# Kernel tuning notes

Measured on AMD Instinct MI355X. Metric: run time of the kernel, lower is better.

The kernel has to match this reference:

```python
import jax, jax.numpy as jnp
import numpy as np

FEAT_DIM = 128
TIME_DIM = 128
D_MODEL = FEAT_DIM + TIME_DIM  # 256
N_HEAD = 2
D_K = D_MODEL // N_HEAD  # 128
B, N = 4096, 64


def setup_inputs() -> dict:
    key = jax.random.key(0)
    ks = jax.random.split(key, 16)
    s = lambda k, sh, sc=0.05: jax.random.normal(k, sh, dtype=jnp.float32) * sc
    return {
        "src": jax.random.normal(ks[0], (B, FEAT_DIM), dtype=jnp.float32),
        "src_t": jax.random.normal(ks[1], (B, 1, TIME_DIM), dtype=jnp.float32),
        "seq": jax.random.normal(ks[2], (B, N, FEAT_DIM), dtype=jnp.float32),
        "seq_t": jax.random.normal(ks[3], (B, N, TIME_DIM), dtype=jnp.float32),
        "mask": jax.random.randint(ks[4], (B, N), 0, 2).astype(jnp.bool_),
        # attention params (x @ W convention, W: [d_model, n_head*d_k])
        "w_qs": s(ks[5], (D_MODEL, N_HEAD * D_K)),
        "w_ks": s(ks[6], (D_MODEL, N_HEAD * D_K)),
        "w_vs": s(ks[7], (D_MODEL, N_HEAD * D_K)),
        "fc_w": s(ks[8], (N_HEAD * D_K, D_MODEL)),
        "fc_b": jnp.zeros((D_MODEL,), jnp.float32),
        "ln_g": jnp.ones((D_MODEL,), jnp.float32),
        "ln_b": jnp.zeros((D_MODEL,), jnp.float32),
        # MergeLayer params: fc1 [(d_model+feat), feat], fc2 [feat, feat]
        "fc1_w": s(ks[9], (D_MODEL + FEAT_DIM, FEAT_DIM)),
        "fc1_b": jnp.zeros((FEAT_DIM,), jnp.float32),
        "fc2_w": s(ks[10], (FEAT_DIM, FEAT_DIM)),
        "fc2_b": jnp.zeros((FEAT_DIM,), jnp.float32),
    }


def _layer_norm(x, g, b, eps=1e-5):
    mu = jnp.mean(x, axis=-1, keepdims=True)
    var = jnp.mean((x - mu) ** 2, axis=-1, keepdims=True)
    return (x - mu) * jax.lax.rsqrt(var + eps) * g + b


def reference(src, src_t, seq, seq_t, mask,
              w_qs, w_ks, w_vs, fc_w, fc_b, ln_g, ln_b,
              fc1_w, fc1_b, fc2_w, fc2_b):
    # q: [B,1,D_MODEL] = cat(src, src_t); k=v: [B,N,D_MODEL]
    q_in = jnp.concatenate([src[:, None, :], src_t], axis=2)
    k_in = jnp.concatenate([seq, seq_t], axis=2)

    q = (q_in @ w_qs).reshape(B, 1, N_HEAD, D_K)   # [B,1,H,dk]
    k = (k_in @ w_ks).reshape(B, N, N_HEAD, D_K)   # [B,N,H,dk]
    v = (k_in @ w_vs).reshape(B, N, N_HEAD, D_K)   # [B,N,H,dv]

    # scaled dot-product attention, len_q == 1
    attn = jnp.einsum('bqhd,bkhd->bhqk', q, k) / jnp.sqrt(jnp.float32(D_K))
    attn = jnp.where(mask[:, None, None, :], jnp.float32(-1e10), attn)
    attn = jax.nn.softmax(attn, axis=-1)           # [B,H,1,N]

    out = jnp.einsum('bhqk,bkhd->bqhd', attn, v).reshape(B, 1, N_HEAD * D_K)
    out = out @ fc_w + fc_b                         # dropout is identity (eval)
    out = _layer_norm(out + q_in, ln_g, ln_b)       # [B,1,D_MODEL]

    out = out[:, 0, :]                              # squeeze -> [B,D_MODEL]
    # MergeLayer: cat(out, src) -> fc1 -> relu -> fc2
    h = jnp.concatenate([out, src], axis=1)
    h = jax.nn.relu(h @ fc1_w + fc1_b)
    merged = h @ fc2_w + fc2_b                      # [B, FEAT_DIM]

    # attn squeeze: [n_head*B, N] ordering matches torch view(n_head, B, ...)
    attn_sq = jnp.transpose(attn[:, :, 0, :], (1, 0, 2)).reshape(N_HEAD * B, N)
    return merged, attn_sq
```

## Files before the change

### kernel.cpp

```cpp
#include <hip/hip_runtime.h>


__device__ __forceinline__ void fma4(float4& a, float s, const float4& w) {
  a.x = fmaf(s, w.x, a.x); a.y = fmaf(s, w.y, a.y);
  a.z = fmaf(s, w.z, a.z); a.w = fmaf(s, w.w, a.w);
}
__device__ __forceinline__ float dot4(const float4& a, const float4& b) {
  return a.x * b.x + a.y * b.y + a.z * b.z + a.w * b.w;
}

__global__ __launch_bounds__(256) void k_wf(const float* __restrict__ w_qs,
                                            const float* __restrict__ w_ks,
                                            float* __restrict__ W) {
  const int idx = blockIdx.x * 256 + threadIdx.x;
  const int c = idx >> 9;
  const int col = idx & 511;
  const int h = col >> 8;
  const int j = col & 255;
  const float* a = w_qs + c * 256 + h * 128;
  const float* bk = w_ks + j * 256 + h * 128;
  float acc = 0.f;
#pragma unroll
  for (int d = 0; d < 128; d += 4)
    acc += dot4(*(const float4*)&a[d], *(const float4*)&bk[d]);
  W[idx] = acc * 0.08838834764831845f;
}

__global__ __launch_bounds__(256) void k_qk(const float* __restrict__ src,
                                            const float* __restrict__ srct,
                                            const float* __restrict__ W,
                                            float* __restrict__ QK) {
  __shared__ float sQ[16 * 256];
  const int tid = threadIdx.x;
  const int rb = (blockIdx.x >> 1) * 16;
  const int ch = (blockIdx.x & 1) * 256;
  {
    const int r = tid >> 4;
    const int cb = (tid & 15) * 16;
#pragma unroll
    for (int i = 0; i < 4; ++i) {
      const int c = cb + i * 4;
      float4 v = (c < 128) ? *(const float4*)&src[(rb + r) * 128 + c]
                           : *(const float4*)&srct[(rb + r) * 128 + (c - 128)];
      *(float4*)&sQ[r * 256 + c] = v;
    }
  }
  __syncthreads();
  const int rg = tid >> 6;
  const int cg = tid & 63;
  const int col = ch + cg * 4;
  float4 acc[4] = {};
  for (int k = 0; k < 256; k += 4) {
    const float4 w0 = *(const float4*)&W[(k + 0) * 512 + col];
    const float4 w1 = *(const float4*)&W[(k + 1) * 512 + col];
    const float4 w2 = *(const float4*)&W[(k + 2) * 512 + col];
    const float4 w3 = *(const float4*)&W[(k + 3) * 512 + col];
#pragma unroll
    for (int r = 0; r < 4; ++r) {
      const float4 a = *(const float4*)&sQ[(rg * 4 + r) * 256 + k];
      fma4(acc[r], a.x, w0); fma4(acc[r], a.y, w1);
      fma4(acc[r], a.z, w2); fma4(acc[r], a.w, w3);
    }
  }
#pragma unroll
  for (int r = 0; r < 4; ++r)
    *(float4*)&QK[(rb + rg * 4 + r) * 512 + col] = acc[r];
}

__global__ __launch_bounds__(256) void k_attn(const float* __restrict__ seq,
                                              const float* __restrict__ seqt,
                                              const unsigned int* __restrict__ mw,
                                              float* QKS,
                                              float* __restrict__ att) {
  __shared__ float sqk[512];
  __shared__ float part0[4][64];
  __shared__ float part1[4][64];
  __shared__ float sa0[64];
  __shared__ float sa1[64];
  __shared__ int nlist[64];
  const int tid = threadIdx.x;
  const int lane = tid & 63;
  const int w = tid >> 6;
  const int b = blockIdx.x;

  if (tid < 128)
    *(float4*)&sqk[tid * 4] = *(const float4*)&QKS[b * 512 + tid * 4];
  const bool masked = (mw[b * 64 + lane] != 0u);
  __syncthreads();

  const float* rowp = (w < 2) ? (seq + b * 8192 + lane * 128 + w * 64)
                              : (seqt + b * 8192 + lane * 128 + (w - 2) * 64);
  float p0 = 0.f, p1 = 0.f;
  if (!masked) {
    const float* q0 = &sqk[w * 64];
    const float* q1 = &sqk[256 + w * 64];
#pragma unroll 8
    for (int i = 0; i < 16; ++i) {
      const float4 kv = *(const float4*)&rowp[i * 4];
      p0 += dot4(kv, *(const float4*)&q0[i * 4]);
      p1 += dot4(kv, *(const float4*)&q1[i * 4]);
    }
  }
  part0[w][lane] = p0;
  part1[w][lane] = p1;
  __syncthreads();

  const float fp0 =
      part0[0][lane] + part0[1][lane] + part0[2][lane] + part0[3][lane];
  const float fp1 =
      part1[0][lane] + part1[1][lane] + part1[2][lane] + part1[3][lane];
  const float e0 = masked ? 0.f : __expf(fp0);
  const float e1 = masked ? 0.f : __expf(fp1);
  float l0 = e0, l1 = e1;
#pragma unroll
  for (int off = 32; off >= 1; off >>= 1) {
    l0 += __shfl_xor(l0, off);
    l1 += __shfl_xor(l1, off);
  }
  const float a0 = e0 / l0;
  const float a1 = e1 / l1;
  const unsigned long long bits = __ballot(!masked);
  if (w == 0) {
    att[b * 64 + lane] = a0;
    att[4096 * 64 + b * 64 + lane] = a1;
    sa0[lane] = a0;
    sa1[lane] = a1;
    const int pos = __popcll(bits & ((1ull << lane) - 1ull));
    if (!masked) nlist[pos] = lane;
  }
  __syncthreads();

  const int cnt = __popcll(bits);
  const float* kin2 = (w < 2) ? (seq + b * 8192 + w * 64 + lane)
                              : (seqt + b * 8192 + (w - 2) * 64 + lane);
  float s0 = 0.f, s1 = 0.f;
  int t = 0;
  for (; t + 4 <= cnt; t += 4) {
    const int n0 = nlist[t + 0];
    const int n1 = nlist[t + 1];
    const int n2 = nlist[t + 2];
    const int n3 = nlist[t + 3];
    const float k0 = kin2[n0 * 128];
    const float k1 = kin2[n1 * 128];
    const float k2 = kin2[n2 * 128];
    const float k3 = kin2[n3 * 128];
    s0 = fmaf(sa0[n0], k0, s0); s1 = fmaf(sa1[n0], k0, s1);
    s0 = fmaf(sa0[n1], k1, s0); s1 = fmaf(sa1[n1], k1, s1);
    s0 = fmaf(sa0[n2], k2, s0); s1 = fmaf(sa1[n2], k2, s1);
    s0 = fmaf(sa0[n3], k3, s0); s1 = fmaf(sa1[n3], k3, s1);
  }
  for (; t < cnt; ++t) {
    const int n = nlist[t];
    const float kv = kin2[n * 128];
    s0 = fmaf(sa0[n], kv, s0);
    s1 = fmaf(sa1[n], kv, s1);
  }
  QKS[b * 512 + w * 64 + lane] = s0;
  QKS[b * 512 + 256 + w * 64 + lane] = s1;
}

__global__ __launch_bounds__(256) void k_epi(
    const float* __restrict__ S, const float* __restrict__ src,
    const float* __restrict__ srct, const float* __restrict__ w_vs,
    const float* __restrict__ fc_w, const float* __restrict__ fc_b,
    const float* __restrict__ ln_g, const float* __restrict__ ln_b,
    const float* __restrict__ fc1_w, const float* __restrict__ fc1_b,
    const float* __restrict__ fc2_w, const float* __restrict__ fc2_b,
    float* __restrict__ out) {
  __shared__ float sv[4][512];
  __shared__ float qin[4][256];
  __shared__ float ov[4][256];
  __shared__ float hcat[4][384];
  __shared__ float h1[4][128];
  __shared__ float red[4][4][2];
  const int tid = threadIdx.x;
  const int lane = tid & 63;
  const int wv = tid >> 6;
  const int b0 = blockIdx.x * 4;

#pragma unroll
  for (int i = 0; i < 2; ++i) {
    const int f4 = i * 256 + tid;
    const int g = f4 >> 7;
    const int c = (f4 & 127) * 4;
    *(float4*)&sv[g][c] = *(const float4*)&S[(b0 + g) * 512 + c];
  }
  {
    const int g = tid >> 6;
    const int c = (tid & 63) * 4;
    float4 v = (c < 128) ? *(const float4*)&src[(b0 + g) * 128 + c]
                         : *(const float4*)&srct[(b0 + g) * 128 + (c - 128)];
    *(float4*)&qin[g][c] = v;
  }
  __syncthreads();

  const int h = tid >> 7;
  {
    float acc[4] = {0.f, 0.f, 0.f, 0.f};
    for (int t = 0; t < 256; t += 4) {
      const float w0 = w_vs[(t + 0) * 256 + tid];
      const float w1 = w_vs[(t + 1) * 256 + tid];
      const float w2 = w_vs[(t + 2) * 256 + tid];
      const float w3 = w_vs[(t + 3) * 256 + tid];
#pragma unroll
      for (int g = 0; g < 4; ++g) {
        const float4 s4 = *(const float4*)&sv[g][h * 256 + t];
        acc[g] = fmaf(s4.x, w0, acc[g]);
        acc[g] = fmaf(s4.y, w1, acc[g]);
        acc[g] = fmaf(s4.z, w2, acc[g]);
        acc[g] = fmaf(s4.w, w3, acc[g]);
      }
    }
#pragma unroll
    for (int g = 0; g < 4; ++g) ov[g][tid] = acc[g];
  }
  __syncthreads();

  float x[4];
  {
    float acc[4] = {0.f, 0.f, 0.f, 0.f};
    for (int d = 0; d < 256; d += 4) {
      const float w0 = fc_w[(d + 0) * 256 + tid];
      const float w1 = fc_w[(d + 1) * 256 + tid];
      const float w2 = fc_w[(d + 2) * 256 + tid];
      const float w3 = fc_w[(d + 3) * 256 + tid];
#pragma unroll
      for (int g = 0; g < 4; ++g) {
        const float4 o4 = *(const float4*)&ov[g][d];
        acc[g] = fmaf(o4.x, w0, acc[g]);
        acc[g] = fmaf(o4.y, w1, acc[g]);
        acc[g] = fmaf(o4.z, w2, acc[g]);
        acc[g] = fmaf(o4.w, w3, acc[g]);
      }
    }
    const float fb = fc_b[tid];
#pragma unroll
    for (int g = 0; g < 4; ++g) x[g] = acc[g] + fb + qin[g][tid];
  }

#pragma unroll
  for (int g = 0; g < 4; ++g) {
    float s = x[g];
    float q = x[g] * x[g];
#pragma unroll
    for (int off = 32; off >= 1; off >>= 1) {
      s += __shfl_xor(s, off);
      q += __shfl_xor(q, off);
    }
    if (lane == 0) {
      red[wv][g][0] = s;
      red[wv][g][1] = q;
    }
  }
  __syncthreads();
  {
    const float gg = ln_g[tid], bb = ln_b[tid];
#pragma unroll
    for (int g = 0; g < 4; ++g) {
      const float s = red[0][g][0] + red[1][g][0] + red[2][g][0] + red[3][g][0];
      const float q = red[0][g][1] + red[1][g][1] + red[2][g][1] + red[3][g][1];
      const float mu = s * (1.0f / 256.0f);
      const float rstd = rsqrtf(q * (1.0f / 256.0f) - mu * mu + 1e-5f);
      hcat[g][tid] = (x[g] - mu) * rstd * gg + bb;
    }
  }
#pragma unroll
  for (int i = 0; i < 2; ++i) {
    const int idx = i * 256 + tid;
    const int g = idx >> 7, c = idx & 127;
    hcat[g][256 + c] = qin[g][c];
  }
  __syncthreads();

  {
    const int col = tid & 127;
    const int gp = (tid >> 7) * 2;
    float acc0 = fc1_b[col], acc1 = acc0;
    for (int d = 0; d < 384; d += 4) {
      const float w0 = fc1_w[(d + 0) * 128 + col];
      const float w1 = fc1_w[(d + 1) * 128 + col];
      const float w2 = fc1_w[(d + 2) * 128 + col];
      const float w3 = fc1_w[(d + 3) * 128 + col];
      const float4 a4 = *(const float4*)&hcat[gp][d];
      const float4 b4 = *(const float4*)&hcat[gp + 1][d];
      acc0 = fmaf(a4.x, w0, acc0); acc0 = fmaf(a4.y, w1, acc0);
      acc0 = fmaf(a4.z, w2, acc0); acc0 = fmaf(a4.w, w3, acc0);
      acc1 = fmaf(b4.x, w0, acc1); acc1 = fmaf(b4.y, w1, acc1);
      acc1 = fmaf(b4.z, w2, acc1); acc1 = fmaf(b4.w, w3, acc1);
    }
    h1[gp][col] = fmaxf(acc0, 0.f);
    h1[gp + 1][col] = fmaxf(acc1, 0.f);
  }
  __syncthreads();

  {
    const int col = tid & 127;
    const int gp = (tid >> 7) * 2;
    float acc0 = fc2_b[col], acc1 = acc0;
    for (int d = 0; d < 128; d += 4) {
      const float w0 = fc2_w[(d + 0) * 128 + col];
      const float w1 = fc2_w[(d + 1) * 128 + col];
      const float w2 = fc2_w[(d + 2) * 128 + col];
      const float w3 = fc2_w[(d + 3) * 128 + col];
      const float4 a4 = *(const float4*)&h1[gp][d];
      const float4 b4 = *(const float4*)&h1[gp + 1][d];
      acc0 = fmaf(a4.x, w0, acc0); acc0 = fmaf(a4.y, w1, acc0);
      acc0 = fmaf(a4.z, w2, acc0); acc0 = fmaf(a4.w, w3, acc0);
      acc1 = fmaf(b4.x, w0, acc1); acc1 = fmaf(b4.y, w1, acc1);
      acc1 = fmaf(b4.z, w2, acc1); acc1 = fmaf(b4.w, w3, acc1);
    }
    out[(b0 + gp) * 128 + col] = acc0;
    out[(b0 + gp + 1) * 128 + col] = acc1;
  }
}

extern "C" void kernel_launch(void* const* d_in, const int* in_sizes, int n_in,
                              void* d_out, int out_size, void* d_ws,
                              size_t ws_size, hipStream_t stream) {
  (void)in_sizes; (void)n_in; (void)out_size; (void)ws_size;
  const float* src = (const float*)d_in[0];
  const float* srct = (const float*)d_in[1];
  const float* seq = (const float*)d_in[2];
  const float* seqt = (const float*)d_in[3];
  const unsigned int* mask = (const unsigned int*)d_in[4];
  const float* w_qs = (const float*)d_in[5];
  const float* w_ks = (const float*)d_in[6];
  const float* w_vs = (const float*)d_in[7];
  const float* fc_w = (const float*)d_in[8];
  const float* fc_b = (const float*)d_in[9];
  const float* ln_g = (const float*)d_in[10];
  const float* ln_b = (const float*)d_in[11];
  const float* fc1_w = (const float*)d_in[12];
  const float* fc1_b = (const float*)d_in[13];
  const float* fc2_w = (const float*)d_in[14];
  const float* fc2_b = (const float*)d_in[15];
  float* out = (float*)d_out;
  float* att = out + 4096 * 128;
  float* W = (float*)d_ws;
  float* QKS = W + 256 * 512;
  k_wf<<<512, 256, 0, stream>>>(w_qs, w_ks, W);
  k_qk<<<512, 256, 0, stream>>>(src, srct, W, QKS);
  k_attn<<<4096, 256, 0, stream>>>(seq, seqt, mask, QKS, att);
  k_epi<<<1024, 256, 0, stream>>>(QKS, src, srct, w_vs, fc_w, fc_b, ln_g,
                                  ln_b, fc1_w, fc1_b, fc2_w, fc2_b, out);
}
```

Before: 384.5 us.

## Precompute w_vs·fc_w product, keep K rows in registers, batch 8 rows in epilogue

The prep kernel now also forms M = per-head w_vs times fc_w, so the epilogue applies one 512x256 matrix instead of two chained GEMMs. The attention kernel keeps its 64-float slice of each key row in registers and computes the weighted sum with shuffle reductions and a shared-memory combine. This replaces the second gather pass over seq/seqt, which reread the key data from global memory. The epilogue handles 8 batch rows per block, doubling weight reuse per block, at the cost of more registers and shared memory (64 kv floats per thread in attention, about 30KB LDS in the epilogue) and possible occupancy loss.

```diff
diff --git a/kernel.cpp b/kernel.cpp
--- a/kernel.cpp
+++ b/kernel.cpp
@@ -9,21 +9,41 @@
   return a.x * b.x + a.y * b.y + a.z * b.z + a.w * b.w;
 }
 
-__global__ __launch_bounds__(256) void k_wf(const float* __restrict__ w_qs,
-                                            const float* __restrict__ w_ks,
-                                            float* __restrict__ W) {
-  const int idx = blockIdx.x * 256 + threadIdx.x;
-  const int c = idx >> 9;
-  const int col = idx & 511;
-  const int h = col >> 8;
-  const int j = col & 255;
-  const float* a = w_qs + c * 256 + h * 128;
-  const float* bk = w_ks + j * 256 + h * 128;
-  float acc = 0.f;
-#pragma unroll
-  for (int d = 0; d < 128; d += 4)
-    acc += dot4(*(const float4*)&a[d], *(const float4*)&bk[d]);
-  W[idx] = acc * 0.08838834764831845f;
+__global__ __launch_bounds__(256) void k_prep(const float* __restrict__ w_qs,
+                                              const float* __restrict__ w_ks,
+                                              const float* __restrict__ w_vs,
+                                              const float* __restrict__ fc_w,
+                                              float* __restrict__ W,
+                                              float* __restrict__ M) {
+  const int bid = blockIdx.x;
+  const int tid = threadIdx.x;
+  if (bid < 512) {
+    const int idx = bid * 256 + tid;
+    const int c = idx >> 9;
+    const int col = idx & 511;
+    const int h = col >> 8;
+    const int j = col & 255;
+    const float* a = w_qs + c * 256 + h * 128;
+    const float* bk = w_ks + j * 256 + h * 128;
+    float acc = 0.f;
+#pragma unroll
+    for (int d = 0; d < 128; d += 4)
+      acc += dot4(*(const float4*)&a[d], *(const float4*)&bk[d]);
+    W[idx] = acc * 0.08838834764831845f;
+  } else {
+    const int u = bid - 512;
+    const int h = u >> 8, t = u & 255;
+    const float* wv = w_vs + t * 256 + h * 128;
+    const float* fw = fc_w + (h * 128) * 256;
+    float acc = 0.f;
+    for (int jj = 0; jj < 128; jj += 4) {
+      acc = fmaf(wv[jj + 0], fw[(jj + 0) * 256 + tid], acc);
+      acc = fmaf(wv[jj + 1], fw[(jj + 1) * 256 + tid], acc);
+      acc = fmaf(wv[jj + 2], fw[(jj + 2) * 256 + tid], acc);
+      acc = fmaf(wv[jj + 3], fw[(jj + 3) * 256 + tid], acc);
+    }
+    M[u * 256 + tid] = acc;
+  }
 }
 
 __global__ __launch_bounds__(256) void k_qk(const float* __restrict__ src,
@@ -75,9 +95,7 @@
   __shared__ float sqk[512];
   __shared__ float part0[4][64];
   __shared__ float part1[4][64];
-  __shared__ float sa0[64];
-  __shared__ float sa1[64];
-  __shared__ int nlist[64];
+  __shared__ float sp[2][4][4][68];
   const int tid = threadIdx.x;
   const int lane = tid & 63;
   const int w = tid >> 6;
@@ -90,15 +108,18 @@
 
   const float* rowp = (w < 2) ? (seq + b * 8192 + lane * 128 + w * 64)
                               : (seqt + b * 8192 + lane * 128 + (w - 2) * 64);
+  float4 kv[16];
+#pragma unroll
+  for (int i = 0; i < 16; ++i) kv[i] = make_float4(0.f, 0.f, 0.f, 0.f);
   float p0 = 0.f, p1 = 0.f;
   if (!masked) {
     const float* q0 = &sqk[w * 64];
     const float* q1 = &sqk[256 + w * 64];
-#pragma unroll 8
+#pragma unroll
     for (int i = 0; i < 16; ++i) {
-      const float4 kv = *(const float4*)&rowp[i * 4];
-      p0 += dot4(kv, *(const float4*)&q0[i * 4]);
-      p1 += dot4(kv, *(const float4*)&q1[i * 4]);
+      kv[i] = *(const float4*)&rowp[i * 4];
+      p0 += dot4(kv[i], *(const float4*)&q0[i * 4]);
+      p1 += dot4(kv[i], *(const float4*)&q1[i * 4]);
     }
   }
   part0[w][lane] = p0;
@@ -119,127 +140,103 @@
   }
   const float a0 = e0 / l0;
   const float a1 = e1 / l1;
-  const unsigned long long bits = __ballot(!masked);
   if (w == 0) {
     att[b * 64 + lane] = a0;
     att[4096 * 64 + b * 64 + lane] = a1;
-    sa0[lane] = a0;
-    sa1[lane] = a1;
-    const int pos = __popcll(bits & ((1ull << lane) - 1ull));
-    if (!masked) nlist[pos] = lane;
-  }
-  __syncthreads();
-
-  const int cnt = __popcll(bits);
-  const float* kin2 = (w < 2) ? (seq + b * 8192 + w * 64 + lane)
-                              : (seqt + b * 8192 + (w - 2) * 64 + lane);
-  float s0 = 0.f, s1 = 0.f;
-  int t = 0;
-  for (; t + 4 <= cnt; t += 4) {
-    const int n0 = nlist[t + 0];
-    const int n1 = nlist[t + 1];
-    const int n2 = nlist[t + 2];
-    const int n3 = nlist[t + 3];
-    const float k0 = kin2[n0 * 128];
-    const float k1 = kin2[n1 * 128];
-    const float k2 = kin2[n2 * 128];
-    const float k3 = kin2[n3 * 128];
-    s0 = fmaf(sa0[n0], k0, s0); s1 = fmaf(sa1[n0], k0, s1);
-    s0 = fmaf(sa0[n1], k1, s0); s1 = fmaf(sa1[n1], k1, s1);
-    s0 = fmaf(sa0[n2], k2, s0); s1 = fmaf(sa1[n2], k2, s1);
-    s0 = fmaf(sa0[n3], k3, s0); s1 = fmaf(sa1[n3], k3, s1);
-  }
-  for (; t < cnt; ++t) {
-    const int n = nlist[t];
-    const float kv = kin2[n * 128];
-    s0 = fmaf(sa0[n], kv, s0);
-    s1 = fmaf(sa1[n], kv, s1);
-  }
-  QKS[b * 512 + w * 64 + lane] = s0;
-  QKS[b * 512 + 256 + w * 64 + lane] = s1;
+  }
+
+  const int g = lane >> 4;
+#pragma unroll
+  for (int i = 0; i < 16; ++i) {
+    float4 t0, t1;
+    t0.x = kv[i].x * a0; t0.y = kv[i].y * a0;
+    t0.z = kv[i].z * a0; t0.w = kv[i].w * a0;
+    t1.x = kv[i].x * a1; t1.y = kv[i].y * a1;
+    t1.z = kv[i].z * a1; t1.w = kv[i].w * a1;
+#pragma unroll
+    for (int off = 1; off <= 8; off <<= 1) {
+      t0.x += __shfl_xor(t0.x, off); t0.y += __shfl_xor(t0.y, off);
+      t0.z += __shfl_xor(t0.z, off); t0.w += __shfl_xor(t0.w, off);
+      t1.x += __shfl_xor(t1.x, off); t1.y += __shfl_xor(t1.y, off);
+      t1.z += __shfl_xor(t1.z, off); t1.w += __shfl_xor(t1.w, off);
+    }
+    if ((lane & 15) == 0) {
+      *(float4*)&sp[0][w][g][i * 4] = t0;
+      *(float4*)&sp[1][w][g][i * 4] = t1;
+    }
+  }
+  __syncthreads();
+
+  {
+    const int wo = tid >> 6, j = tid & 63;
+    const float s0 =
+        sp[0][wo][0][j] + sp[0][wo][1][j] + sp[0][wo][2][j] + sp[0][wo][3][j];
+    const float s1 =
+        sp[1][wo][0][j] + sp[1][wo][1][j] + sp[1][wo][2][j] + sp[1][wo][3][j];
+    QKS[b * 512 + wo * 64 + j] = s0;
+    QKS[b * 512 + 256 + wo * 64 + j] = s1;
+  }
 }
 
 __global__ __launch_bounds__(256) void k_epi(
     const float* __restrict__ S, const float* __restrict__ src,
-    const float* __restrict__ srct, const float* __restrict__ w_vs,
-    const float* __restrict__ fc_w, const float* __restrict__ fc_b,
-    const float* __restrict__ ln_g, const float* __restrict__ ln_b,
-    const float* __restrict__ fc1_w, const float* __restrict__ fc1_b,
-    const float* __restrict__ fc2_w, const float* __restrict__ fc2_b,
-    float* __restrict__ out) {
-  __shared__ float sv[4][512];
-  __shared__ float qin[4][256];
-  __shared__ float ov[4][256];
-  __shared__ float hcat[4][384];
-  __shared__ float h1[4][128];
-  __shared__ float red[4][4][2];
+    const float* __restrict__ srct, const float* __restrict__ M,
+    const float* __restrict__ fc_b, const float* __restrict__ ln_g,
+    const float* __restrict__ ln_b, const float* __restrict__ fc1_w,
+    const float* __restrict__ fc1_b, const float* __restrict__ fc2_w,
+    const float* __restrict__ fc2_b, float* __restrict__ out) {
+  __shared__ float sv[8][512];
+  __shared__ float qin[8][256];
+  __shared__ float hcat[8][384];
+  __shared__ float h1[8][128];
+  __shared__ float red[4][8][2];
   const int tid = threadIdx.x;
   const int lane = tid & 63;
   const int wv = tid >> 6;
-  const int b0 = blockIdx.x * 4;
-
-#pragma unroll
-  for (int i = 0; i < 2; ++i) {
+  const int b0 = blockIdx.x * 8;
+
+#pragma unroll
+  for (int i = 0; i < 4; ++i) {
     const int f4 = i * 256 + tid;
     const int g = f4 >> 7;
     const int c = (f4 & 127) * 4;
     *(float4*)&sv[g][c] = *(const float4*)&S[(b0 + g) * 512 + c];
   }
-  {
-    const int g = tid >> 6;
-    const int c = (tid & 63) * 4;
+#pragma unroll
+  for (int i = 0; i < 2; ++i) {
+    const int f4 = i * 256 + tid;
+    const int g = f4 >> 6;
+    const int c = (f4 & 63) * 4;
     float4 v = (c < 128) ? *(const float4*)&src[(b0 + g) * 128 + c]
                          : *(const float4*)&srct[(b0 + g) * 128 + (c - 128)];
     *(float4*)&qin[g][c] = v;
   }
   __syncthreads();
 
-  const int h = tid >> 7;
-  {
-    float acc[4] = {0.f, 0.f, 0.f, 0.f};
-    for (int t = 0; t < 256; t += 4) {
-      const float w0 = w_vs[(t + 0) * 256 + tid];
-      const float w1 = w_vs[(t + 1) * 256 + tid];
-      const float w2 = w_vs[(t + 2) * 256 + tid];
-      const float w3 = w_vs[(t + 3) * 256 + tid];
-#pragma unroll
-      for (int g = 0; g < 4; ++g) {
-        const float4 s4 = *(const float4*)&sv[g][h * 256 + t];
+  float x[8];
+  {
+    float acc[8] = {};
+    for (int d = 0; d < 512; d += 4) {
+      const float w0 = M[(d + 0) * 256 + tid];
+      const float w1 = M[(d + 1) * 256 + tid];
+      const float w2 = M[(d + 2) * 256 + tid];
+      const float w3 = M[(d + 3) * 256 + tid];
+#pragma unroll
+      for (int g = 0; g < 8; ++g) {
+        const float4 s4 = *(const float4*)&sv[g][d];
         acc[g] = fmaf(s4.x, w0, acc[g]);
         acc[g] = fmaf(s4.y, w1, acc[g]);
         acc[g] = fmaf(s4.z, w2, acc[g]);
         acc[g] = fmaf(s4.w, w3, acc[g]);
       }
     }
-#pragma unroll
-    for (int g = 0; g < 4; ++g) ov[g][tid] = acc[g];
-  }
-  __syncthreads();
-
-  float x[4];
-  {
-    float acc[4] = {0.f, 0.f, 0.f, 0.f};
-    for (int d = 0; d < 256; d += 4) {
-      const float w0 = fc_w[(d + 0) * 256 + tid];
-      const float w1 = fc_w[(d + 1) * 256 + tid];
-      const float w2 = fc_w[(d + 2) * 256 + tid];
-      const float w3 = fc_w[(d + 3) * 256 + tid];
-#pragma unroll
-      for (int g = 0; g < 4; ++g) {
-        const float4 o4 = *(const float4*)&ov[g][d];
-        acc[g] = fmaf(o4.x, w0, acc[g]);
-        acc[g] = fmaf(o4.y, w1, acc[g]);
-        acc[g] = fmaf(o4.z, w2, acc[g]);
-        acc[g] = fmaf(o4.w, w3, acc[g]);
-      }
-    }
     const float fb = fc_b[tid];
 #pragma unroll
-    for (int g = 0; g < 4; ++g) x[g] = acc[g] + fb + qin[g][tid];
-  }
-
-#pragma unroll
-  for (int g = 0; g < 4; ++g) {
+    for (int g = 0; g < 8; ++g) x[g] = acc[g] + fb + qin[g][tid];
+  }
+
+#pragma unroll
+  for (int g = 0; g < 8; ++g) {
     float s = x[g];
     float q = x[g] * x[g];
 #pragma unroll
@@ -256,7 +253,7 @@
   {
     const float gg = ln_g[tid], bb = ln_b[tid];
 #pragma unroll
-    for (int g = 0; g < 4; ++g) {
+    for (int g = 0; g < 8; ++g) {
       const float s = red[0][g][0] + red[1][g][0] + red[2][g][0] + red[3][g][0];
       const float q = red[0][g][1] + red[1][g][1] + red[2][g][1] + red[3][g][1];
       const float mu = s * (1.0f / 256.0f);
@@ -265,7 +262,7 @@
     }
   }
 #pragma unroll
-  for (int i = 0; i < 2; ++i) {
+  for (int i = 0; i < 4; ++i) {
     const int idx = i * 256 + tid;
     const int g = idx >> 7, c = idx & 127;
     hcat[g][256 + c] = qin[g][c];
@@ -274,8 +271,8 @@
 
   {
     const int col = tid & 127;
-    const int gp = (tid >> 7) * 2;
-    float acc0 = fc1_b[col], acc1 = acc0;
+    const int gp = (tid >> 7) * 4;
+    float acc0 = fc1_b[col], acc1 = acc0, acc2 = acc0, acc3 = acc0;
     for (int d = 0; d < 384; d += 4) {
       const float w0 = fc1_w[(d + 0) * 128 + col];
       const float w1 = fc1_w[(d + 1) * 128 + col];
@@ -283,20 +280,28 @@
       const float w3 = fc1_w[(d + 3) * 128 + col];
       const float4 a4 = *(const float4*)&hcat[gp][d];
       const float4 b4 = *(const float4*)&hcat[gp + 1][d];
+      const float4 c4 = *(const float4*)&hcat[gp + 2][d];
+      const float4 d4 = *(const float4*)&hcat[gp + 3][d];
       acc0 = fmaf(a4.x, w0, acc0); acc0 = fmaf(a4.y, w1, acc0);
       acc0 = fmaf(a4.z, w2, acc0); acc0 = fmaf(a4.w, w3, acc0);
       acc1 = fmaf(b4.x, w0, acc1); acc1 = fmaf(b4.y, w1, acc1);
       acc1 = fmaf(b4.z, w2, acc1); acc1 = fmaf(b4.w, w3, acc1);
+      acc2 = fmaf(c4.x, w0, acc2); acc2 = fmaf(c4.y, w1, acc2);
+      acc2 = fmaf(c4.z, w2, acc2); acc2 = fmaf(c4.w, w3, acc2);
+      acc3 = fmaf(d4.x, w0, acc3); acc3 = fmaf(d4.y, w1, acc3);
+      acc3 = fmaf(d4.z, w2, acc3); acc3 = fmaf(d4.w, w3, acc3);
     }
     h1[gp][col] = fmaxf(acc0, 0.f);
     h1[gp + 1][col] = fmaxf(acc1, 0.f);
+    h1[gp + 2][col] = fmaxf(acc2, 0.f);
+    h1[gp + 3][col] = fmaxf(acc3, 0.f);
   }
   __syncthreads();
 
   {
     const int col = tid & 127;
-    const int gp = (tid >> 7) * 2;
-    float acc0 = fc2_b[col], acc1 = acc0;
+    const int gp = (tid >> 7) * 4;
+    float acc0 = fc2_b[col], acc1 = acc0, acc2 = acc0, acc3 = acc0;
     for (int d = 0; d < 128; d += 4) {
       const float w0 = fc2_w[(d + 0) * 128 + col];
       const float w1 = fc2_w[(d + 1) * 128 + col];
@@ -304,13 +309,21 @@
       const float w3 = fc2_w[(d + 3) * 128 + col];
       const float4 a4 = *(const float4*)&h1[gp][d];
       const float4 b4 = *(const float4*)&h1[gp + 1][d];
+      const float4 c4 = *(const float4*)&h1[gp + 2][d];
+      const float4 d4 = *(const float4*)&h1[gp + 3][d];
       acc0 = fmaf(a4.x, w0, acc0); acc0 = fmaf(a4.y, w1, acc0);
       acc0 = fmaf(a4.z, w2, acc0); acc0 = fmaf(a4.w, w3, acc0);
       acc1 = fmaf(b4.x, w0, acc1); acc1 = fmaf(b4.y, w1, acc1);
       acc1 = fmaf(b4.z, w2, acc1); acc1 = fmaf(b4.w, w3, acc1);
+      acc2 = fmaf(c4.x, w0, acc2); acc2 = fmaf(c4.y, w1, acc2);
+      acc2 = fmaf(c4.z, w2, acc2); acc2 = fmaf(c4.w, w3, acc2);
+      acc3 = fmaf(d4.x, w0, acc3); acc3 = fmaf(d4.y, w1, acc3);
+      acc3 = fmaf(d4.z, w2, acc3); acc3 = fmaf(d4.w, w3, acc3);
     }
     out[(b0 + gp) * 128 + col] = acc0;
     out[(b0 + gp + 1) * 128 + col] = acc1;
+    out[(b0 + gp + 2) * 128 + col] = acc2;
+    out[(b0 + gp + 3) * 128 + col] = acc3;
   }
 }
 
@@ -337,10 +350,11 @@
   float* out = (float*)d_out;
   float* att = out + 4096 * 128;
   float* W = (float*)d_ws;
-  float* QKS = W + 256 * 512;
-  k_wf<<<512, 256, 0, stream>>>(w_qs, w_ks, W);
+  float* M = W + 256 * 512;
+  float* QKS = M + 512 * 256;
+  k_prep<<<1024, 256, 0, stream>>>(w_qs, w_ks, w_vs, fc_w, W, M);
   k_qk<<<512, 256, 0, stream>>>(src, srct, W, QKS);
   k_attn<<<4096, 256, 0, stream>>>(seq, seqt, mask, QKS, att);
-  k_epi<<<1024, 256, 0, stream>>>(QKS, src, srct, w_vs, fc_w, fc_b, ln_g,
-                                  ln_b, fc1_w, fc1_b, fc2_w, fc2_b, out);
-}
+  k_epi<<<512, 256, 0, stream>>>(QKS, src, srct, M, fc_b, ln_g, ln_b, fc1_w,
+                                 fc1_b, fc2_w, fc2_b, out);
+}
```

Result: slower. 438.4 us (+14.0%).
